# Optimization experiments

Hardware: AMD Instinct MI355X
Metric: run time of the kernel (lower is better)

The kernel has to match this reference:

```python
import jax, jax.numpy as jnp
import numpy as np
from jax import lax

B, N, H, K = 2, 128, 768, 64          # batch, pad_size, bert hidden, num_clusters
H2, H3, H4, NC = 256, 128, 32, 7      # gcn hidden sizes, num_classes
FC1, FC2 = 1000, 100


def setup_inputs() -> dict:
    key = jax.random.key(0)
    ks = jax.random.split(key, 16)
    rn = lambda k, shape, s=0.02: (jax.random.normal(k, shape, jnp.float32) * s)
    return {
        "encoder_out": jax.random.normal(ks[0], (B, N, H), jnp.float32),
        "mask": jnp.ones((B, N), jnp.float32),
        "landmarks": jax.random.normal(ks[1], (K, H), jnp.float32),
        "d": jnp.array([0.3], jnp.float32),
        "alpha": jnp.array([0.5], jnp.float32),
        "beta": jnp.array([1.0], jnp.float32),
        "gcn_w1": rn(ks[2], (H, H2)), "gcn_b1": jnp.zeros((H2,), jnp.float32),
        "gcn_w2": rn(ks[3], (H2, H3)), "gcn_b2": jnp.zeros((H3,), jnp.float32),
        "gcn_w3": rn(ks[4], (H3, H4)), "gcn_b3": jnp.zeros((H4,), jnp.float32),
        "adj_w": rn(ks[5], (H4, H)), "adj_b": jnp.zeros((H,), jnp.float32),
        "fc1_w": rn(ks[6], (H * K, FC1)), "fc1_b": jnp.zeros((FC1,), jnp.float32),
        "fc2_w": rn(ks[7], (FC1, FC2)), "fc2_b": jnp.zeros((FC2,), jnp.float32),
        "fc3_w": rn(ks[8], (FC2, NC)), "fc3_b": jnp.zeros((NC,), jnp.float32),
    }


def _forward(encoder_out, mask, landmarks, d, alpha, beta,
             gcn_w1, gcn_b1, gcn_w2, gcn_b2, gcn_w3, gcn_b3,
             adj_w, adj_b, fc1_w, fc1_b, fc2_w, fc2_b, fc3_w, fc3_b):
    eps = 1e-6
    # distance_matrix: [B,N,K], min-max normalized over cluster dim
    diff = encoder_out[:, :, None, :] - landmarks[None, None, :, :]   # [B,N,K,H]
    dist = jnp.sqrt(jnp.sum(diff * diff, axis=-1))                    # [B,N,K]
    mn = dist.min(axis=-1, keepdims=True)
    mx = dist.max(axis=-1, keepdims=True)
    dist = (dist - mn) / (mx - mn + eps)

    # probability_matrix: gaussian similarity, mask tokens, normalize over token dim
    sim = jnp.exp(-dist ** 2 / (2.0 * d[0] ** 2)) * mask[:, :, None]  # [B,N,K]
    P = sim / (sim.sum(axis=1, keepdims=True) + eps)                  # [B,N,K]

    # distance weight over token positions: exp(-alpha * |i-j|)  [N,N]
    idx = jnp.arange(N)
    Wd = jnp.exp(-alpha[0] * jnp.abs(idx[:, None] - idx[None, :]).astype(jnp.float32))

    # graph_constructing on P^T [B,K,N]: G[b,i,j] = sum_{k,l} exp(beta*p[b,i,k]*p[b,j,l]*Wd[k,l]) - 1
    p = jnp.transpose(P, (0, 2, 1))                                   # [B,K,N]
    outer = jnp.einsum('bik,bjl->bijkl', p, p)                        # [B,K,K,N,N]
    Q = jnp.exp(beta[0] * outer * Wd[None, None, None]) - 1.0
    G = Q.sum(axis=(-1, -2))                                          # [B,K,K]
    # weight graph only feeds edge_index (nonzero pattern) in the torch model -> non-differentiable
    G = lax.stop_gradient(G)

    # node features: P^T @ encoder_out  -> [B,K,H]
    node_feat = jnp.einsum('bnk,bnh->bkh', P, encoder_out)

    # GCNConv adjacency: binary nonzero pattern + remaining self-loops, sym-normalized
    eye = jnp.eye(K, dtype=bool)
    A = (G != 0).astype(jnp.float32)
    A = jnp.where(eye[None], 1.0, A)
    deg = A.sum(axis=-1)                                              # [B,K]
    dinv = jnp.where(deg > 0, 1.0 / jnp.sqrt(deg), 0.0)
    nadj = dinv[:, :, None] * A * dinv[:, None, :]                    # [B,K,K]

    h = jax.nn.relu(jnp.einsum('bij,bjd->bid', nadj, node_feat @ gcn_w1) + gcn_b1)
    h = jax.nn.relu(jnp.einsum('bij,bjd->bid', nadj, h @ gcn_w2) + gcn_b2)
    h = jax.nn.relu(jnp.einsum('bij,bjd->bid', nadj, h @ gcn_w3) + gcn_b3)  # [B,K,32]
    out = h @ adj_w + adj_b + node_feat                               # residual [B,K,H]

    x = out.reshape(B, K * H)
    x = jax.nn.gelu(x @ fc1_w + fc1_b, approximate=False)
    x = jax.nn.gelu(x @ fc2_w + fc2_b, approximate=False)
    return x @ fc3_w + fc3_b                                          # [B,NC]


def reference(encoder_out, mask, landmarks, d, alpha, beta,
              gcn_w1, gcn_b1, gcn_w2, gcn_b2, gcn_w3, gcn_b3,
              adj_w, adj_b, fc1_w, fc1_b, fc2_w, fc2_b, fc3_w, fc3_b):
    return _forward(encoder_out, mask, landmarks, d, alpha, beta,
                    gcn_w1, gcn_b1, gcn_w2, gcn_b2, gcn_w3, gcn_b3,
                    adj_w, adj_b, fc1_w, fc1_b, fc2_w, fc2_b, fc3_w, fc3_b)
```

## Files before the change

### kernel.cpp

```cpp
#include <hip/hip_runtime.h>
#include <hip/hip_bf16.h>
#include <math.h>

#define BB 2
#define NN 128
#define HH 768
#define KK 64
#define H2 256
#define H3 128
#define H4 32
#define NC 7
#define FC1N 1000
#define FC2N 100

#define SPLIT 256
#define HBLK 192

__device__ __forceinline__ float gelu_exact(float x) {
    return 0.5f * x * (1.0f + erff(x * 0.70710678118654752f));
}

__global__ void __launch_bounds__(256) k_dist(const float* __restrict__ enc,
                                              const float* __restrict__ mask,
                                              const float* __restrict__ lm,
                                              const float* __restrict__ dptr,
                                              float* __restrict__ pT) {
    __shared__ __align__(16) float es[HH];
    __shared__ float pd[4][KK];
    int blk = blockIdx.x;
    int b = blk >> 7, n = blk & 127;
    int t = threadIdx.x;
    const float4* erow4 = reinterpret_cast<const float4*>(enc + ((size_t)b * NN + n) * HH);
    if (t < HH / 4) reinterpret_cast<float4*>(es)[t] = erow4[t];
    __syncthreads();
    int k = t & 63, part = t >> 6;
    const float4* l4 = reinterpret_cast<const float4*>(lm + (size_t)k * HH + part * 192);
    const float4* e4 = reinterpret_cast<const float4*>(es + part * 192);
    float s = 0.f;
    #pragma unroll 8
    for (int h = 0; h < 48; ++h) {
        float4 a = e4[h], w = l4[h];
        float d0 = a.x - w.x, d1 = a.y - w.y, d2 = a.z - w.z, d3 = a.w - w.w;
        s += d0 * d0 + d1 * d1 + d2 * d2 + d3 * d3;
    }
    pd[part][k] = s;
    __syncthreads();
    if (t < 64) {
        float d2 = pd[0][t] + pd[1][t] + pd[2][t] + pd[3][t];
        float dist = sqrtf(d2);
        float mn = dist, mx = dist;
        for (int o = 32; o; o >>= 1) {
            mn = fminf(mn, __shfl_xor(mn, o));
            mx = fmaxf(mx, __shfl_xor(mx, o));
        }
        float dn = (dist - mn) / (mx - mn + 1e-6f);
        float dval = dptr[0];
        float sim = expf(-(dn * dn) / (2.0f * dval * dval)) * mask[b * NN + n];
        pT[((size_t)b * KK + t) * NN + n] = sim;
    }
}

__global__ void k_pnorm(float* __restrict__ pT) {
    int row = blockIdx.x;
    int t = threadIdx.x;
    float* r = pT + (size_t)row * NN;
    float v0 = r[t], v1 = r[t + 64];
    float s = v0 + v1;
    for (int o = 32; o; o >>= 1) s += __shfl_xor(s, o);
    float den = s + 1e-6f;
    r[t] = v0 / den;
    r[t + 64] = v1 / den;
}

__global__ void __launch_bounds__(256) k_graph(const float* __restrict__ pT,
                                               const float* __restrict__ aptr,
                                               const float* __restrict__ bptr,
                                               float* __restrict__ G) {
    int blk = blockIdx.x;
    int b = blk >> 12;
    int i = (blk >> 6) & 63, j = blk & 63;
    if (i > j) return;
    __shared__ float wvx[256], pi[NN], pj[NN];
    __shared__ float red[4];
    int t = threadIdx.x;
    float alpha = aptr[0], beta = bptr[0];
    wvx[t] = __expf(-alpha * fabsf((float)(t - 128)));
    if (t < 128) pi[t] = pT[((size_t)b * KK + i) * NN + t];
    else         pj[t - 128] = pT[((size_t)b * KK + j) * NN + (t - 128)];
    __syncthreads();
    int tt = t & 127;
    int s0 = t >> 7;
    float pjv = pj[tt] * beta;
    const float* wp = wvx + (128 + s0 - tt);
    float acc = 0.f;
    #pragma unroll
    for (int it = 0; it < 64; ++it) {
        int s = s0 + 2 * it;
        acc += __expf(pjv * pi[s] * wp[2 * it]);
    }
    acc -= 64.0f;
    for (int o = 32; o; o >>= 1) acc += __shfl_xor(acc, o);
    if ((t & 63) == 0) red[t >> 6] = acc;
    __syncthreads();
    if (t == 0) {
        float total = red[0] + red[1] + red[2] + red[3];
        G[((size_t)b * KK + i) * KK + j] = total;
        G[((size_t)b * KK + j) * KK + i] = total;
    }
}

__global__ void k_nadj(const float* __restrict__ G, float* __restrict__ nadj) {
    __shared__ float dinv[KK];
    int b = blockIdx.x;
    int i = threadIdx.x;
    const float* gr = G + ((size_t)b * KK + i) * KK;
    float deg = 0.f;
    for (int j = 0; j < KK; ++j) {
        float a = (j == i) ? 1.f : ((gr[j] != 0.f) ? 1.f : 0.f);
        deg += a;
    }
    dinv[i] = (deg > 0.f) ? (1.0f / sqrtf(deg)) : 0.f;
    __syncthreads();
    float di = dinv[i];
    float* nr = nadj + ((size_t)b * KK + i) * KK;
    for (int j = 0; j < KK; ++j) {
        float a = (j == i) ? 1.f : ((gr[j] != 0.f) ? 1.f : 0.f);
        nr[j] = di * a * dinv[j];
    }
}

__global__ void __launch_bounds__(256) k_nodefeat(const float* __restrict__ pT,
                                                  const float* __restrict__ enc,
                                                  float* __restrict__ nf) {
    __shared__ float pr[NN];
    int blk = blockIdx.x;
    int b = blk >> 6;
    int t = threadIdx.x;
    if (t < NN) pr[t] = pT[(size_t)blk * NN + t];
    __syncthreads();
    const float* eb = enc + (size_t)b * NN * HH;
    float a0 = 0.f, a1 = 0.f, a2 = 0.f;
    for (int n = 0; n < NN; ++n) {
        float p = pr[n];
        const float* er = eb + (size_t)n * HH;
        a0 += p * er[t];
        a1 += p * er[t + 256];
        a2 += p * er[t + 512];
    }
    float* o = nf + (size_t)blk * HH;
    o[t] = a0; o[t + 256] = a1; o[t + 512] = a2;
}

template<int Hd, int Jd>
__global__ void k_mm4v(const float* __restrict__ X, const float* __restrict__ W,
                       float* __restrict__ O) {
    __shared__ __align__(16) float s[4 * Hd];
    int m0 = blockIdx.x * 4;
    for (int idx = threadIdx.x; idx < Hd; idx += blockDim.x)
        reinterpret_cast<float4*>(s)[idx] =
            reinterpret_cast<const float4*>(X + (size_t)m0 * Hd)[idx];
    __syncthreads();
    int r  = threadIdx.x / (Jd / 4);
    int jg = threadIdx.x % (Jd / 4);
    const float* xr = s + r * Hd;
    const float4* W4 = reinterpret_cast<const float4*>(W) + jg;
    float4 acc = {0.f, 0.f, 0.f, 0.f};
    #pragma unroll 4
    for (int h = 0; h < Hd; ++h) {
        float4 w = W4[(size_t)h * (Jd / 4)];
        float x = xr[h];
        acc.x += x * w.x; acc.y += x * w.y; acc.z += x * w.z; acc.w += x * w.w;
    }
    reinterpret_cast<float4*>(O + (size_t)(m0 + r) * Jd)[jg] = acc;
}

template<int Jd>
__global__ void k_adjrelu(const float* __restrict__ nadj, const float* __restrict__ X,
                          const float* __restrict__ bias, float* __restrict__ O) {
    __shared__ float ar[KK];
    int blk = blockIdx.x;
    int b = blk >> 6;
    for (int idx = threadIdx.x; idx < KK; idx += blockDim.x)
        ar[idx] = nadj[(size_t)blk * KK + idx];
    __syncthreads();
    int t = threadIdx.x;
    const float4* xb4 = reinterpret_cast<const float4*>(X + (size_t)b * KK * Jd) + t;
    float4 acc = reinterpret_cast<const float4*>(bias)[t];
    #pragma unroll 8
    for (int jj = 0; jj < KK; ++jj) {
        float a = ar[jj];
        float4 x = xb4[(size_t)jj * (Jd / 4)];
        acc.x += a * x.x; acc.y += a * x.y; acc.z += a * x.z; acc.w += a * x.w;
    }
    acc.x = fmaxf(acc.x, 0.f); acc.y = fmaxf(acc.y, 0.f);
    acc.z = fmaxf(acc.z, 0.f); acc.w = fmaxf(acc.w, 0.f);
    reinterpret_cast<float4*>(O + (size_t)blk * Jd)[t] = acc;
}

__global__ void __launch_bounds__(256) k_fc1(const float* __restrict__ h3,
                                             const float* __restrict__ adj_w,
                                             const float* __restrict__ adj_b,
                                             const float* __restrict__ nf,
                                             const float* __restrict__ W,
                                             float* __restrict__ part) {
    __shared__ __align__(16) float xs[2 * HBLK];
    __shared__ float h3s[2][H4];
    int s = blockIdx.x;
    int krow = s >> 2;
    int c0 = (s & 3) * HBLK;
    int t = threadIdx.x;
    if (t < 2 * H4) h3s[t >> 5][t & 31] = h3[(size_t)((t >> 5) * KK + krow) * H4 + (t & 31)];
    __syncthreads();
    for (int idx = t; idx < 2 * HBLK; idx += 256) {
        int bb = idx / HBLK, h = idx - bb * HBLK;
        int hcol = c0 + h;
        float acc = adj_b[hcol] + nf[(size_t)(bb * KK + krow) * HH + hcol];
        #pragma unroll
        for (int kk = 0; kk < H4; ++kk) acc += h3s[bb][kk] * adj_w[(size_t)kk * HH + hcol];
        xs[idx] = acc;
    }
    __syncthreads();
    if (t < 250) {
        float4 a0 = {0.f, 0.f, 0.f, 0.f}, a1 = {0.f, 0.f, 0.f, 0.f};
        const float4* W4 = reinterpret_cast<const float4*>(W) + t;
        int h0 = s * HBLK;
        for (int hh = 0; hh < HBLK; ++hh) {
            float4 w = W4[(size_t)(h0 + hh) * 250];
            float x0 = xs[hh], x1 = xs[HBLK + hh];
            a0.x += x0 * w.x; a0.y += x0 * w.y; a0.z += x0 * w.z; a0.w += x0 * w.w;
            a1.x += x1 * w.x; a1.y += x1 * w.y; a1.z += x1 * w.z; a1.w += x1 * w.w;
        }
        float* p0 = part + (size_t)s * (2 * FC1N);
        reinterpret_cast<float4*>(p0)[t] = a0;
        reinterpret_cast<float4*>(p0 + FC1N)[t] = a1;
    }
}

__global__ void k_fc1red(const float* __restrict__ part, const float* __restrict__ bias,
                         float* __restrict__ y1) {
    int g = blockIdx.x * 256 + threadIdx.x;
    if (g >= 2 * FC1N) return;
    int b = g / FC1N, j = g % FC1N;
    float acc = bias[j];
    for (int s = 0; s < SPLIT; ++s) acc += part[(size_t)s * (2 * FC1N) + b * FC1N + j];
    y1[g] = gelu_exact(acc);
}

__global__ void __launch_bounds__(512) k_fc23(const float* __restrict__ y1,
                                              const float* __restrict__ W2,
                                              const float* __restrict__ b2,
                                              const float* __restrict__ W3,
                                              const float* __restrict__ b3,
                                              float* __restrict__ out) {
    __shared__ float ys[2 * FC1N];
    __shared__ float psum[4][2][128];
    __shared__ float y2s[2][FC2N];
    int t = threadIdx.x;
    for (int idx = t; idx < 2 * FC1N; idx += 512) ys[idx] = y1[idx];
    __syncthreads();
    int j = t & 127, kp = t >> 7;
    float a0 = 0.f, a1 = 0.f;
    if (j < FC2N) {
        const float* ya = ys + kp * 250;
        const float* yb = ys + FC1N + kp * 250;
        const float* wp = W2 + (size_t)(kp * 250) * FC2N + j;
        #pragma unroll 4
        for (int h = 0; h < 250; ++h) {
            float w = wp[(size_t)h * FC2N];
            a0 += ya[h] * w;
            a1 += yb[h] * w;
        }
    }
    psum[kp][0][j] = a0;
    psum[kp][1][j] = a1;
    __syncthreads();
    if (t < 2 * FC2N) {
        int bb = t / FC2N, jj = t % FC2N;
        float acc = b2[jj] + psum[0][bb][jj] + psum[1][bb][jj]
                  + psum[2][bb][jj] + psum[3][bb][jj];
        y2s[bb][jj] = gelu_exact(acc);
    }
    __syncthreads();
    if (t < BB * NC) {
        int bb = t / NC, c = t % NC;
        float acc = b3[c];
        for (int h = 0; h < FC2N; ++h) acc += y2s[bb][h] * W3[h * NC + c];
        out[t] = acc;
    }
}

extern "C" void kernel_launch(void* const* d_in, const int* in_sizes, int n_in,
                              void* d_out, int out_size, void* d_ws, size_t ws_size,
                              hipStream_t stream) {
    const float* enc   = (const float*)d_in[0];
    const float* mask  = (const float*)d_in[1];
    const float* lm    = (const float*)d_in[2];
    const float* dptr  = (const float*)d_in[3];
    const float* aptr  = (const float*)d_in[4];
    const float* bptr  = (const float*)d_in[5];
    const float* w1    = (const float*)d_in[6];
    const float* b1    = (const float*)d_in[7];
    const float* w2    = (const float*)d_in[8];
    const float* b2    = (const float*)d_in[9];
    const float* w3    = (const float*)d_in[10];
    const float* b3    = (const float*)d_in[11];
    const float* adj_w = (const float*)d_in[12];
    const float* adj_b = (const float*)d_in[13];
    const float* fc1w  = (const float*)d_in[14];
    const float* fc1b  = (const float*)d_in[15];
    const float* fc2w  = (const float*)d_in[16];
    const float* fc2b  = (const float*)d_in[17];
    const float* fc3w  = (const float*)d_in[18];
    const float* fc3b  = (const float*)d_in[19];
    float* out = (float*)d_out;

    float* w = (float*)d_ws;
    float* pT   = w;
    float* G    = pT + 16384;
    float* nadj = G + 8192;
    float* nf   = nadj + 8192;
    float* xw1  = nf + 98304;
    float* h1   = xw1 + 32768;
    float* xw2  = h1 + 32768;
    float* h2   = xw2 + 16384;
    float* xw3  = h2 + 16384;
    float* h3   = xw3 + 4096;
    float* part = h3 + 4096;
    float* y1   = part + 512000;

    k_dist<<<BB * NN, 256, 0, stream>>>(enc, mask, lm, dptr, pT);
    k_pnorm<<<BB * KK, 64, 0, stream>>>(pT);
    k_graph<<<BB * KK * KK, 256, 0, stream>>>(pT, aptr, bptr, G);
    k_nadj<<<BB, 64, 0, stream>>>(G, nadj);
    k_nodefeat<<<BB * KK, 256, 0, stream>>>(pT, enc, nf);
    k_mm4v<HH, H2><<<32, H2, 0, stream>>>(nf, w1, xw1);
    k_adjrelu<H2><<<BB * KK, H2 / 4, 0, stream>>>(nadj, xw1, b1, h1);
    k_mm4v<H2, H3><<<32, H3, 0, stream>>>(h1, w2, xw2);
    k_adjrelu<H3><<<BB * KK, H3 / 4, 0, stream>>>(nadj, xw2, b2, h2);
    k_mm4v<H3, H4><<<32, H4, 0, stream>>>(h2, w3, xw3);
    k_adjrelu<H4><<<BB * KK, H4 / 4, 0, stream>>>(nadj, xw3, b3, h3);
    k_fc1<<<SPLIT, 256, 0, stream>>>(h3, adj_w, adj_b, nf, fc1w, part);
    k_fc1red<<<8, 256, 0, stream>>>(part, fc1b, y1);
    k_fc23<<<1, 512, 0, stream>>>(y1, fc2w, fc2b, fc3w, fc3b, out);
}
```

Measured before the change: 598.9 us.

## Fold P normalization into consumers, split-K GCN matmuls, fuse third GCN layer

Drops the separate P-normalization kernel. The token-sum denominator is now recomputed inside the graph and node-feature kernels and applied as a scale. The GCN feature matmuls become split-K with 4 partial slices summed inside the adjacency-relu kernel, giving more blocks. The small third GCN layer (matmul plus adjacency plus relu) is fused into one kernel, and the fc1 split count is doubled with a smaller per-block row slice, adding parallelism at the cost of a larger partial-sum reduction.

Measured after the change: 511.5 us. 14.6% less time.

```diff
diff --git a/kernel.cpp b/kernel.cpp
--- a/kernel.cpp
+++ b/kernel.cpp
@@ -13,8 +13,8 @@
 #define FC1N 1000
 #define FC2N 100
 
-#define SPLIT 256
-#define HBLK 192
+#define SPLIT 512
+#define HBLK 96
 
 __device__ __forceinline__ float gelu_exact(float x) {
     return 0.5f * x * (1.0f + erff(x * 0.70710678118654752f));
@@ -60,18 +60,6 @@
     }
 }
 
-__global__ void k_pnorm(float* __restrict__ pT) {
-    int row = blockIdx.x;
-    int t = threadIdx.x;
-    float* r = pT + (size_t)row * NN;
-    float v0 = r[t], v1 = r[t + 64];
-    float s = v0 + v1;
-    for (int o = 32; o; o >>= 1) s += __shfl_xor(s, o);
-    float den = s + 1e-6f;
-    r[t] = v0 / den;
-    r[t + 64] = v1 / den;
-}
-
 __global__ void __launch_bounds__(256) k_graph(const float* __restrict__ pT,
                                                const float* __restrict__ aptr,
                                                const float* __restrict__ bptr,
@@ -81,16 +69,28 @@
     int i = (blk >> 6) & 63, j = blk & 63;
     if (i > j) return;
     __shared__ float wvx[256], pi[NN], pj[NN];
-    __shared__ float red[4];
+    __shared__ float red[4], dens[2];
     int t = threadIdx.x;
     float alpha = aptr[0], beta = bptr[0];
     wvx[t] = __expf(-alpha * fabsf((float)(t - 128)));
     if (t < 128) pi[t] = pT[((size_t)b * KK + i) * NN + t];
     else         pj[t - 128] = pT[((size_t)b * KK + j) * NN + (t - 128)];
     __syncthreads();
+    if (t < 64) {
+        float s = pi[t] + pi[t + 64];
+        for (int o = 32; o; o >>= 1) s += __shfl_xor(s, o);
+        if (t == 0) dens[0] = s + 1e-6f;
+    } else if (t < 128) {
+        int u = t - 64;
+        float s = pj[u] + pj[u + 64];
+        for (int o = 32; o; o >>= 1) s += __shfl_xor(s, o);
+        if (u == 0) dens[1] = s + 1e-6f;
+    }
+    __syncthreads();
+    float c = beta / (dens[0] * dens[1]);
     int tt = t & 127;
     int s0 = t >> 7;
-    float pjv = pj[tt] * beta;
+    float pjv = pj[tt] * c;
     const float* wp = wvx + (128 + s0 - tt);
     float acc = 0.f;
     #pragma unroll
@@ -107,6 +107,37 @@
         G[((size_t)b * KK + i) * KK + j] = total;
         G[((size_t)b * KK + j) * KK + i] = total;
     }
+}
+
+__global__ void __launch_bounds__(256) k_nodefeat(const float* __restrict__ pT,
+                                                  const float* __restrict__ enc,
+                                                  float* __restrict__ nf) {
+    __shared__ float pr[NN];
+    __shared__ float dsh;
+    int blk = blockIdx.x;
+    int b = blk >> 6;
+    int t = threadIdx.x;
+    if (t < NN) pr[t] = pT[(size_t)blk * NN + t];
+    __syncthreads();
+    if (t < 64) {
+        float s = pr[t] + pr[t + 64];
+        for (int o = 32; o; o >>= 1) s += __shfl_xor(s, o);
+        if (t == 0) dsh = s + 1e-6f;
+    }
+    __syncthreads();
+    float inv = 1.0f / dsh;
+    const float* eb = enc + (size_t)b * NN * HH;
+    float a0 = 0.f, a1 = 0.f, a2 = 0.f;
+    #pragma unroll 8
+    for (int n = 0; n < NN; ++n) {
+        float p = pr[n];
+        const float* er = eb + (size_t)n * HH;
+        a0 += p * er[t];
+        a1 += p * er[t + 256];
+        a2 += p * er[t + 512];
+    }
+    float* o = nf + (size_t)blk * HH;
+    o[t] = a0 * inv; o[t + 256] = a1 * inv; o[t + 512] = a2 * inv;
 }
 
 __global__ void k_nadj(const float* __restrict__ G, float* __restrict__ nadj) {
@@ -129,54 +160,37 @@
     }
 }
 
-__global__ void __launch_bounds__(256) k_nodefeat(const float* __restrict__ pT,
-                                                  const float* __restrict__ enc,
-                                                  float* __restrict__ nf) {
-    __shared__ float pr[NN];
+template<int Hd, int Jd, int KP>
+__global__ void k_mmks(const float* __restrict__ X, const float* __restrict__ W,
+                       float* __restrict__ part) {
+    const int SLICE = Hd / KP;
+    __shared__ float xs[4][SLICE];
     int blk = blockIdx.x;
-    int b = blk >> 6;
-    int t = threadIdx.x;
-    if (t < NN) pr[t] = pT[(size_t)blk * NN + t];
-    __syncthreads();
-    const float* eb = enc + (size_t)b * NN * HH;
-    float a0 = 0.f, a1 = 0.f, a2 = 0.f;
-    for (int n = 0; n < NN; ++n) {
-        float p = pr[n];
-        const float* er = eb + (size_t)n * HH;
-        a0 += p * er[t];
-        a1 += p * er[t + 256];
-        a2 += p * er[t + 512];
-    }
-    float* o = nf + (size_t)blk * HH;
-    o[t] = a0; o[t + 256] = a1; o[t + 512] = a2;
-}
-
-template<int Hd, int Jd>
-__global__ void k_mm4v(const float* __restrict__ X, const float* __restrict__ W,
-                       float* __restrict__ O) {
-    __shared__ __align__(16) float s[4 * Hd];
-    int m0 = blockIdx.x * 4;
-    for (int idx = threadIdx.x; idx < Hd; idx += blockDim.x)
-        reinterpret_cast<float4*>(s)[idx] =
-            reinterpret_cast<const float4*>(X + (size_t)m0 * Hd)[idx];
-    __syncthreads();
-    int r  = threadIdx.x / (Jd / 4);
-    int jg = threadIdx.x % (Jd / 4);
-    const float* xr = s + r * Hd;
-    const float4* W4 = reinterpret_cast<const float4*>(W) + jg;
-    float4 acc = {0.f, 0.f, 0.f, 0.f};
-    #pragma unroll 4
-    for (int h = 0; h < Hd; ++h) {
-        float4 w = W4[(size_t)h * (Jd / 4)];
-        float x = xr[h];
-        acc.x += x * w.x; acc.y += x * w.y; acc.z += x * w.z; acc.w += x * w.w;
-    }
-    reinterpret_cast<float4*>(O + (size_t)(m0 + r) * Jd)[jg] = acc;
-}
-
-template<int Jd>
-__global__ void k_adjrelu(const float* __restrict__ nadj, const float* __restrict__ X,
-                          const float* __restrict__ bias, float* __restrict__ O) {
+    int mq = blk & 31, p = blk >> 5;
+    int m0 = mq * 4;
+    int h0 = p * SLICE;
+    for (int idx = threadIdx.x; idx < 4 * SLICE; idx += Jd) {
+        int r = idx / SLICE, h = idx - r * SLICE;
+        xs[r][h] = X[(size_t)(m0 + r) * Hd + h0 + h];
+    }
+    __syncthreads();
+    int j = threadIdx.x;
+    float a0 = 0.f, a1 = 0.f, a2 = 0.f, a3 = 0.f;
+    #pragma unroll 32
+    for (int h = 0; h < SLICE; ++h) {
+        float w = W[(size_t)(h0 + h) * Jd + j];
+        a0 += xs[0][h] * w;
+        a1 += xs[1][h] * w;
+        a2 += xs[2][h] * w;
+        a3 += xs[3][h] * w;
+    }
+    float* o = part + (size_t)p * (128 * Jd) + (size_t)m0 * Jd + j;
+    o[0] = a0; o[Jd] = a1; o[2 * Jd] = a2; o[3 * Jd] = a3;
+}
+
+template<int Jd, int KP>
+__global__ void k_adjreluP(const float* __restrict__ nadj, const float* __restrict__ part,
+                           const float* __restrict__ bias, float* __restrict__ O) {
     __shared__ float ar[KK];
     int blk = blockIdx.x;
     int b = blk >> 6;
@@ -184,17 +198,82 @@
         ar[idx] = nadj[(size_t)blk * KK + idx];
     __syncthreads();
     int t = threadIdx.x;
-    const float4* xb4 = reinterpret_cast<const float4*>(X + (size_t)b * KK * Jd) + t;
+    const float4* P4 = reinterpret_cast<const float4*>(part);
     float4 acc = reinterpret_cast<const float4*>(bias)[t];
-    #pragma unroll 8
-    for (int jj = 0; jj < KK; ++jj) {
-        float a = ar[jj];
-        float4 x = xb4[(size_t)jj * (Jd / 4)];
-        acc.x += a * x.x; acc.y += a * x.y; acc.z += a * x.z; acc.w += a * x.w;
+    #pragma unroll
+    for (int p = 0; p < KP; ++p) {
+        #pragma unroll 8
+        for (int jj = 0; jj < KK; ++jj) {
+            float a = ar[jj];
+            float4 x = P4[(size_t)(p * 128 + b * KK + jj) * (Jd / 4) + t];
+            acc.x += a * x.x; acc.y += a * x.y; acc.z += a * x.z; acc.w += a * x.w;
+        }
     }
     acc.x = fmaxf(acc.x, 0.f); acc.y = fmaxf(acc.y, 0.f);
     acc.z = fmaxf(acc.z, 0.f); acc.w = fmaxf(acc.w, 0.f);
     reinterpret_cast<float4*>(O + (size_t)blk * Jd)[t] = acc;
+}
+
+__global__ void __launch_bounds__(256) k_g3a3(const float* __restrict__ h2,
+                                              const float* __restrict__ w3,
+                                              const float* __restrict__ b3,
+                                              const float* __restrict__ nadj,
+                                              float* __restrict__ h3) {
+    __shared__ float h2s[64][129];
+    __shared__ float w3s[128][16];
+    __shared__ float xw3s[64][16];
+    __shared__ float nadjs[64][65];
+    __shared__ float b3s[16];
+    int b = blockIdx.x >> 1, jh = blockIdx.x & 1;
+    int j0 = jh * 16;
+    int t = threadIdx.x;
+    for (int idx = t; idx < 2048; idx += 256) {
+        int r = idx >> 5, c4 = (idx & 31) * 4;
+        float4 v = *reinterpret_cast<const float4*>(h2 + ((size_t)b * KK + r) * H3 + c4);
+        h2s[r][c4] = v.x; h2s[r][c4 + 1] = v.y; h2s[r][c4 + 2] = v.z; h2s[r][c4 + 3] = v.w;
+    }
+    for (int idx = t; idx < 2048; idx += 256) {
+        int kk = idx >> 4, jj = idx & 15;
+        w3s[kk][jj] = w3[(size_t)kk * H4 + j0 + jj];
+    }
+    for (int idx = t; idx < 1024; idx += 256) {
+        int r = idx >> 4, c4 = (idx & 15) * 4;
+        float4 v = *reinterpret_cast<const float4*>(nadj + ((size_t)b * KK + r) * KK + c4);
+        nadjs[r][c4] = v.x; nadjs[r][c4 + 1] = v.y; nadjs[r][c4 + 2] = v.z; nadjs[r][c4 + 3] = v.w;
+    }
+    if (t < 16) b3s[t] = b3[j0 + t];
+    __syncthreads();
+    int j = t & 15, r0 = t >> 4;
+    {
+        float a0 = 0.f, a1 = 0.f, a2 = 0.f, a3 = 0.f;
+        #pragma unroll 8
+        for (int kk = 0; kk < H3; ++kk) {
+            float w = w3s[kk][j];
+            a0 += h2s[r0][kk] * w;
+            a1 += h2s[r0 + 16][kk] * w;
+            a2 += h2s[r0 + 32][kk] * w;
+            a3 += h2s[r0 + 48][kk] * w;
+        }
+        xw3s[r0][j] = a0; xw3s[r0 + 16][j] = a1;
+        xw3s[r0 + 32][j] = a2; xw3s[r0 + 48][j] = a3;
+    }
+    __syncthreads();
+    {
+        float bv = b3s[j];
+        float c0 = bv, c1 = bv, c2 = bv, c3 = bv;
+        #pragma unroll 8
+        for (int jj = 0; jj < KK; ++jj) {
+            float x = xw3s[jj][j];
+            c0 += nadjs[r0][jj] * x;
+            c1 += nadjs[r0 + 16][jj] * x;
+            c2 += nadjs[r0 + 32][jj] * x;
+            c3 += nadjs[r0 + 48][jj] * x;
+        }
+        h3[((size_t)b * KK + r0) * H4 + j0 + j]      = fmaxf(c0, 0.f);
+        h3[((size_t)b * KK + r0 + 16) * H4 + j0 + j] = fmaxf(c1, 0.f);
+        h3[((size_t)b * KK + r0 + 32) * H4 + j0 + j] = fmaxf(c2, 0.f);
+        h3[((size_t)b * KK + r0 + 48) * H4 + j0 + j] = fmaxf(c3, 0.f);
+    }
 }
 
 __global__ void __launch_bounds__(256) k_fc1(const float* __restrict__ h3,
@@ -206,24 +285,25 @@
     __shared__ __align__(16) float xs[2 * HBLK];
     __shared__ float h3s[2][H4];
     int s = blockIdx.x;
-    int krow = s >> 2;
-    int c0 = (s & 3) * HBLK;
+    int krow = s >> 3;
+    int c0 = (s & 7) * HBLK;
     int t = threadIdx.x;
     if (t < 2 * H4) h3s[t >> 5][t & 31] = h3[(size_t)((t >> 5) * KK + krow) * H4 + (t & 31)];
     __syncthreads();
-    for (int idx = t; idx < 2 * HBLK; idx += 256) {
-        int bb = idx / HBLK, h = idx - bb * HBLK;
+    if (t < 2 * HBLK) {
+        int bb = t / HBLK, h = t - bb * HBLK;
         int hcol = c0 + h;
         float acc = adj_b[hcol] + nf[(size_t)(bb * KK + krow) * HH + hcol];
         #pragma unroll
         for (int kk = 0; kk < H4; ++kk) acc += h3s[bb][kk] * adj_w[(size_t)kk * HH + hcol];
-        xs[idx] = acc;
+        xs[t] = acc;
     }
     __syncthreads();
     if (t < 250) {
         float4 a0 = {0.f, 0.f, 0.f, 0.f}, a1 = {0.f, 0.f, 0.f, 0.f};
         const float4* W4 = reinterpret_cast<const float4*>(W) + t;
         int h0 = s * HBLK;
+        #pragma unroll 8
         for (int hh = 0; hh < HBLK; ++hh) {
             float4 w = W4[(size_t)(h0 + hh) * 250];
             float x0 = xs[hh], x1 = xs[HBLK + hh];
@@ -242,6 +322,7 @@
     if (g >= 2 * FC1N) return;
     int b = g / FC1N, j = g % FC1N;
     float acc = bias[j];
+    #pragma unroll 16
     for (int s = 0; s < SPLIT; ++s) acc += part[(size_t)s * (2 * FC1N) + b * FC1N + j];
     y1[g] = gelu_exact(acc);
 }
@@ -315,31 +396,28 @@
     float* out = (float*)d_out;
 
     float* w = (float*)d_ws;
-    float* pT   = w;
-    float* G    = pT + 16384;
-    float* nadj = G + 8192;
-    float* nf   = nadj + 8192;
-    float* xw1  = nf + 98304;
-    float* h1   = xw1 + 32768;
-    float* xw2  = h1 + 32768;
-    float* h2   = xw2 + 16384;
-    float* xw3  = h2 + 16384;
-    float* h3   = xw3 + 4096;
-    float* part = h3 + 4096;
-    float* y1   = part + 512000;
+    float* pT    = w;
+    float* G     = pT + 16384;
+    float* nadj  = G + 8192;
+    float* nf    = nadj + 8192;
+    float* part1 = nf + 98304;
+    float* h1    = part1 + 131072;
+    float* part2 = h1 + 32768;
+    float* h2    = part2 + 65536;
+    float* h3    = h2 + 16384;
+    float* partF = h3 + 4096;
+    float* y1    = partF + 1024000;
 
     k_dist<<<BB * NN, 256, 0, stream>>>(enc, mask, lm, dptr, pT);
-    k_pnorm<<<BB * KK, 64, 0, stream>>>(pT);
     k_graph<<<BB * KK * KK, 256, 0, stream>>>(pT, aptr, bptr, G);
+    k_nodefeat<<<BB * KK, 256, 0, stream>>>(pT, enc, nf);
     k_nadj<<<BB, 64, 0, stream>>>(G, nadj);
-    k_nodefeat<<<BB * KK, 256, 0, stream>>>(pT, enc, nf);
-    k_mm4v<HH, H2><<<32, H2, 0, stream>>>(nf, w1, xw1);
-    k_adjrelu<H2><<<BB * KK, H2 / 4, 0, stream>>>(nadj, xw1, b1, h1);
-    k_mm4v<H2, H3><<<32, H3, 0, stream>>>(h1, w2, xw2);
-    k_adjrelu<H3><<<BB * KK, H3 / 4, 0, stream>>>(nadj, xw2, b2, h2);
-    k_mm4v<H3, H4><<<32, H4, 0, stream>>>(h2, w3, xw3);
-    k_adjrelu<H4><<<BB * KK, H4 / 4, 0, stream>>>(nadj, xw3, b3, h3);
-    k_fc1<<<SPLIT, 256, 0, stream>>>(h3, adj_w, adj_b, nf, fc1w, part);
-    k_fc1red<<<8, 256, 0, stream>>>(part, fc1b, y1);
+    k_mmks<HH, H2, 4><<<128, H2, 0, stream>>>(nf, w1, part1);
+    k_adjreluP<H2, 4><<<BB * KK, H2 / 4, 0, stream>>>(nadj, part1, b1, h1);
+    k_mmks<H2, H3, 4><<<128, H3, 0, stream>>>(h1, w2, part2);
+    k_adjreluP<H3, 4><<<BB * KK, H3 / 4, 0, stream>>>(nadj, part2, b2, h2);
+    k_g3a3<<<4, 256, 0, stream>>>(h2, w3, b3, nadj, h3);
+    k_fc1<<<SPLIT, 256, 0, stream>>>(h3, adj_w, adj_b, nf, fc1w, partF);
+    k_fc1red<<<8, 256, 0, stream>>>(partF, fc1b, y1);
     k_fc23<<<1, 512, 0, stream>>>(y1, fc2w, fc2b, fc3w, fc3b, out);
 }
```
